# Optimization experiments

Measured on AMD Instinct MI355X. Metric: run time of the kernel, lower is better.

## Reference

```python
import jax, jax.numpy as jnp
import numpy as np

NUM_HEADS = 16
D_MODEL = 1024
D_K = D_MODEL // NUM_HEADS
B, S = 2, 2048


def setup_inputs() -> dict:
    key = jax.random.key(0)
    ks = jax.random.split(key, 10)
    q = jax.random.normal(ks[0], (B, S, D_MODEL), dtype=jnp.float32)
    k = jax.random.normal(ks[1], (B, S, D_MODEL), dtype=jnp.float32)
    v = jax.random.normal(ks[2], (B, S, D_MODEL), dtype=jnp.float32)
    # causal mask, 1 = keep, 0 = masked (masked_fill(mask==0, -1e9))
    mask = jnp.tril(jnp.ones((S, S), dtype=jnp.int32))[None, None, :, :]
    # Linear weights ~ N(0, 0.02); biases left at torch default-ish small uniform
    std = 0.02
    Wq = jax.random.normal(ks[3], (D_MODEL, D_MODEL), dtype=jnp.float32) * std
    Wk = jax.random.normal(ks[4], (D_MODEL, D_MODEL), dtype=jnp.float32) * std
    Wv = jax.random.normal(ks[5], (D_MODEL, D_MODEL), dtype=jnp.float32) * std
    bound = 1.0 / np.sqrt(D_MODEL)
    bq = jax.random.uniform(ks[6], (D_MODEL,), jnp.float32, -bound, bound)
    bk = jax.random.uniform(ks[7], (D_MODEL,), jnp.float32, -bound, bound)
    bv = jax.random.uniform(ks[8], (D_MODEL,), jnp.float32, -bound, bound)
    return {"q": q, "k": k, "v": v, "mask": mask,
            "Wq": Wq, "bq": bq, "Wk": Wk, "bk": bk, "Wv": Wv, "bv": bv}


def reference(q, k, v, mask, Wq, bq, Wk, bk, Wv, bv):
    # projections (torch Linear: x @ W.T + b), split heads -> [B, H, S, Dk]
    def proj(x, W, b):
        y = x @ W.T + b
        return y.reshape(B, S, NUM_HEADS, D_K).transpose(0, 2, 1, 3)

    qh, kh, vh = proj(q, Wq, bq), proj(k, Wk, bk), proj(v, Wv, bv)
    scores = jnp.einsum('bhqd,bhkd->bhqk', qh, kh) / jnp.sqrt(jnp.float32(D_K))
    scores = jnp.where(mask == 0, jnp.float32(-1e9), scores)
    p = jax.nn.softmax(scores, axis=-1)
    # dropout is identity in eval mode
    x = jnp.einsum('bhqk,bhkd->bhqd', p, vh)  # [B, H, S, Dk]
    return x.transpose(0, 2, 1, 3).reshape(B, S, D_MODEL)
```

## Files before the change

kernel.cpp:

```cpp
#include <hip/hip_runtime.h>

#define B_ 2
#define H_ 16
#define S_ 2048
#define DM 1024
#define DK 64
#define NX (4096 * 1024)
#define NW (1024 * 1024)

typedef unsigned short u16;
typedef __attribute__((ext_vector_type(8))) short bf16x8;
typedef __attribute__((ext_vector_type(8))) unsigned short u16x8;
typedef __attribute__((ext_vector_type(4))) unsigned short u16x4;
typedef __attribute__((ext_vector_type(4))) float f32x4;

__device__ inline u16 f2bf(float f) {
  union { float f; unsigned int u; } c; c.f = f;
  unsigned int u = c.u;
  u += 0x7fffu + ((u >> 16) & 1u);
  return (u16)(u >> 16);
}

__device__ inline u16x8 cvt8(const float* __restrict__ src) {
  const float4 a = *reinterpret_cast<const float4*>(src);
  const float4 b = *reinterpret_cast<const float4*>(src + 4);
  u16x8 r;
  r[0] = f2bf(a.x); r[1] = f2bf(a.y); r[2] = f2bf(a.z); r[3] = f2bf(a.w);
  r[4] = f2bf(b.x); r[5] = f2bf(b.y); r[6] = f2bf(b.z); r[7] = f2bf(b.w);
  return r;
}

__device__ inline void glds16(const u16* g, u16* l) {
  __builtin_amdgcn_global_load_lds(
      (const __attribute__((address_space(1))) unsigned int*)g,
      (__attribute__((address_space(3))) unsigned int*)l, 16, 0, 0);
}

__global__ __launch_bounds__(256) void cvt_kernel(
    const float* __restrict__ q, const float* __restrict__ k, const float* __restrict__ v,
    const float* __restrict__ Wq, const float* __restrict__ Wk, const float* __restrict__ Wv,
    u16* __restrict__ Xq, u16* __restrict__ Xk, u16* __restrict__ Xv,
    u16* __restrict__ Wqb, u16* __restrict__ Wkb, u16* __restrict__ Wvb)
{
  const int t = blockIdx.y;
  const float* src = (t == 0) ? q : (t == 1) ? k : (t == 2) ? v
                   : (t == 3) ? Wq : (t == 4) ? Wk : Wv;
  u16* dst = (t == 0) ? Xq : (t == 1) ? Xk : (t == 2) ? Xv
           : (t == 3) ? Wqb : (t == 4) ? Wkb : Wvb;
  const int n = (t < 3) ? NX : NW;
  const int idx = (blockIdx.x * 256 + threadIdx.x) * 8;
  if (idx >= n) return;
  *reinterpret_cast<u16x8*>(&dst[idx]) = cvt8(&src[idx]);
}

__global__ __launch_bounds__(256) void proj_kernel(
    const u16* __restrict__ Xq, const u16* __restrict__ Xk, const u16* __restrict__ Xv,
    const u16* __restrict__ Wqb, const u16* __restrict__ Wkb, const u16* __restrict__ Wvb,
    const float* __restrict__ bq, const float* __restrict__ bk, const float* __restrict__ bv,
    u16* __restrict__ Qh, u16* __restrict__ Kh, u16* __restrict__ Vh)
{
  const int z = blockIdx.z;
  const u16* X      = (z == 0) ? Xq : (z == 1) ? Xk : Xv;
  const u16* W      = (z == 0) ? Wqb : (z == 1) ? Wkb : Wvb;
  const float* bias = (z == 0) ? bq : (z == 1) ? bk : bv;
  u16* out          = (z == 0) ? Qh : (z == 1) ? Kh : Vh;
  const float scale = (z == 0) ? 0.125f : 1.0f;

  __shared__ __align__(16) u16 Xs[128 * 32];
  __shared__ __align__(16) u16 Ws[128 * 32];

  const int tid = threadIdx.x;
  const int lane = tid & 63;
  const int w = tid >> 6;
  const int wy = w >> 1, wx = w & 1;
  const int m0 = blockIdx.y * 128;
  const int n0 = blockIdx.x * 128;
  const int ml = lane & 15;
  const int qd = lane >> 4;

  f32x4 acc[4][4] = {};

  for (int kb = 0; kb < DM; kb += 32) {
    __syncthreads();
    #pragma unroll
    for (int p = 0; p < 2; ++p) {
      const int c = p * 4 + w;
      const int row = c * 16 + (lane >> 2);
      const int col = kb + (lane & 3) * 8;
      glds16(&X[(size_t)(m0 + row) * DM + col], &Xs[c * 512]);
      glds16(&W[(size_t)(n0 + row) * DM + col], &Ws[c * 512]);
    }
    __syncthreads();
    bf16x8 a[4], bfr[4];
    #pragma unroll
    for (int i = 0; i < 4; ++i)
      a[i] = *reinterpret_cast<const bf16x8*>(&Xs[(wy * 64 + i * 16 + ml) * 32 + qd * 8]);
    #pragma unroll
    for (int j = 0; j < 4; ++j)
      bfr[j] = *reinterpret_cast<const bf16x8*>(&Ws[(wx * 64 + j * 16 + ml) * 32 + qd * 8]);
    #pragma unroll
    for (int i = 0; i < 4; ++i)
      #pragma unroll
      for (int j = 0; j < 4; ++j)
        acc[i][j] = __builtin_amdgcn_mfma_f32_16x16x32_bf16(a[i], bfr[j], acc[i][j], 0, 0, 0);
  }

  #pragma unroll
  for (int j = 0; j < 4; ++j) {
    const int n = n0 + wx * 64 + j * 16 + ml;
    const float badd = bias[n];
    const int h = n >> 6, d = n & 63;
    #pragma unroll
    for (int i = 0; i < 4; ++i) {
      #pragma unroll
      for (int r = 0; r < 4; ++r) {
        const int m = m0 + wy * 64 + i * 16 + qd * 4 + r;
        const int bi = m >> 11, s = m & 2047;
        out[((bi * H_ + h) * S_ + s) * DK + d] = f2bf((acc[i][j][r] + badd) * scale);
      }
    }
  }
}

__global__ __launch_bounds__(256) void transpose_kernel(
    const u16* __restrict__ Vh, u16* __restrict__ Vt)
{
  __shared__ __align__(16) u16 T[64 * 72];
  const int t = threadIdx.x;
  const int st = blockIdx.x, bh = blockIdx.y;
  {
    const int r = t >> 2, c = (t & 3) * 16;
    const u16* src = &Vh[((size_t)bh * S_ + st * 64 + r) * DK + c];
    *reinterpret_cast<u16x8*>(&T[r * 72 + c])     = *reinterpret_cast<const u16x8*>(src);
    *reinterpret_cast<u16x8*>(&T[r * 72 + c + 8]) = *reinterpret_cast<const u16x8*>(src + 8);
  }
  __syncthreads();
  {
    const int d = t >> 2, s0 = (t & 3) * 16;
    u16x8 a, b;
    #pragma unroll
    for (int i = 0; i < 8; ++i) a[i] = T[(s0 + i) * 72 + d];
    #pragma unroll
    for (int i = 0; i < 8; ++i) b[i] = T[(s0 + 8 + i) * 72 + d];
    u16* dst = &Vt[((size_t)bh * DK + d) * S_ + st * 64 + s0];
    *reinterpret_cast<u16x8*>(dst)     = a;
    *reinterpret_cast<u16x8*>(dst + 8) = b;
  }
}

__global__ __launch_bounds__(256) void attn_kernel(
    const u16* __restrict__ Qh, const u16* __restrict__ Kh,
    const u16* __restrict__ Vt, float* __restrict__ out)
{
  __shared__ __align__(16) u16 Ks[64 * 72];
  __shared__ __align__(16) u16 Vs[64 * 72];
  __shared__ __align__(16) u16 Ps[4 * 16 * 72];

  const int tid  = threadIdx.x;
  const int lane = tid & 63;
  const int w    = tid >> 6;
  const int qt   = (gridDim.x - 1) - blockIdx.x;
  const int bh   = blockIdx.y;
  const int b    = bh >> 4, h = bh & 15;
  const int ml   = lane & 15, qd = lane >> 4;
  const int R0   = qt * 64 + w * 16;

  bf16x8 qa[2];
  #pragma unroll
  for (int ch = 0; ch < 2; ++ch)
    qa[ch] = *reinterpret_cast<const bf16x8*>(
        &Qh[((size_t)bh * S_ + R0 + ml) * DK + ch * 32 + qd * 8]);

  f32x4 oacc[4] = {};
  float l = 0.f;

  const u16* kbase = Kh + (size_t)bh * S_ * DK;
  const u16* vbase = Vt + (size_t)bh * DK * S_;
  u16* pw = &Ps[w * 16 * 72 + ml * 72];

  const int sr = tid >> 3;
  const int sc = (tid & 7) * 8;

  for (int t = 0; t <= qt; ++t) {
    __syncthreads();
    #pragma unroll
    for (int p = 0; p < 2; ++p) {
      const int r = sr + p * 32;
      *reinterpret_cast<float4*>(&Ks[r * 72 + sc]) =
          *reinterpret_cast<const float4*>(&kbase[(size_t)(t * 64 + r) * DK + sc]);
      *reinterpret_cast<float4*>(&Vs[r * 72 + sc]) =
          *reinterpret_cast<const float4*>(&vbase[(size_t)r * S_ + t * 64 + sc]);
    }
    __syncthreads();

    const bool diag = (t == qt);
    const int jmax = diag ? w : 3;

    f32x4 sfr[4];
    #pragma unroll
    for (int j = 0; j < 4; ++j) {
      if (j > jmax) break;
      f32x4 zz = {};
      #pragma unroll
      for (int ch = 0; ch < 2; ++ch) {
        bf16x8 kb = *reinterpret_cast<const bf16x8*>(&Ks[(j * 16 + ml) * 72 + ch * 32 + qd * 8]);
        zz = __builtin_amdgcn_mfma_f32_16x16x32_bf16(kb, qa[ch], zz, 0, 0, 0);
      }
      sfr[j] = zz;
    }

    if (diag) {
      #pragma unroll
      for (int r = 0; r < 4; ++r)
        if (qd * 4 + r > ml) sfr[jmax][r] = -1e30f;
    }

    #pragma unroll
    for (int j = 0; j < 4; ++j) {
      if (j <= jmax) {
        u16x4 pk;
        #pragma unroll
        for (int r = 0; r < 4; ++r) {
          const float e = __expf(sfr[j][r]);
          l += e;
          pk[r] = f2bf(e);
        }
        *reinterpret_cast<u16x4*>(&pw[j * 16 + qd * 4]) = pk;
      } else {
        *reinterpret_cast<u16x4*>(&pw[j * 16 + qd * 4]) = (u16x4){0, 0, 0, 0};
      }
    }

    const int chmax = (diag && w < 2) ? 0 : 1;
    #pragma unroll
    for (int ch = 0; ch < 2; ++ch) {
      if (ch > chmax) break;
      bf16x8 pa = *reinterpret_cast<const bf16x8*>(&Ps[w * 16 * 72 + ml * 72 + ch * 32 + qd * 8]);
      #pragma unroll
      for (int dj = 0; dj < 4; ++dj) {
        bf16x8 vb = *reinterpret_cast<const bf16x8*>(&Vs[(dj * 16 + ml) * 72 + ch * 32 + qd * 8]);
        oacc[dj] = __builtin_amdgcn_mfma_f32_16x16x32_bf16(pa, vb, oacc[dj], 0, 0, 0);
      }
    }
  }

  l += __shfl_xor(l, 16, 64);
  l += __shfl_xor(l, 32, 64);
  float lr[4];
  #pragma unroll
  for (int r = 0; r < 4; ++r) lr[r] = __shfl(l, qd * 4 + r, 64);
  #pragma unroll
  for (int dj = 0; dj < 4; ++dj)
    #pragma unroll
    for (int r = 0; r < 4; ++r) {
      const int srow = R0 + qd * 4 + r;
      out[(size_t)(b * S_ + srow) * DM + h * DK + dj * 16 + ml] = oacc[dj][r] / lr[r];
    }
}

extern "C" void kernel_launch(void* const* d_in, const int* in_sizes, int n_in,
                              void* d_out, int out_size, void* d_ws, size_t ws_size,
                              hipStream_t stream) {
  const float* q  = (const float*)d_in[0];
  const float* k  = (const float*)d_in[1];
  const float* v  = (const float*)d_in[2];
  const float* Wq = (const float*)d_in[4];
  const float* bq = (const float*)d_in[5];
  const float* Wk = (const float*)d_in[6];
  const float* bk = (const float*)d_in[7];
  const float* Wv = (const float*)d_in[8];
  const float* bv = (const float*)d_in[9];

  u16* Xq  = (u16*)d_ws;
  u16* Xk  = Xq + NX;
  u16* Xv  = Xk + NX;
  u16* Wqb = Xv + NX;
  u16* Wkb = Wqb + NW;
  u16* Wvb = Wkb + NW;
  u16* Qh  = Wvb + NW;
  u16* Kh  = Qh + NX;
  u16* Vh  = Kh + NX;
  u16* Vt  = Xq;

  cvt_kernel<<<dim3(NX / (256 * 8), 6), 256, 0, stream>>>(
      q, k, v, Wq, Wk, Wv, Xq, Xk, Xv, Wqb, Wkb, Wvb);
  proj_kernel<<<dim3(DM / 128, (B_ * S_) / 128, 3), 256, 0, stream>>>(
      Xq, Xk, Xv, Wqb, Wkb, Wvb, bq, bk, bv, Qh, Kh, Vh);
  transpose_kernel<<<dim3(S_ / 64, B_ * H_), 256, 0, stream>>>(Vh, Vt);
  attn_kernel<<<dim3(S_ / 64, B_ * H_), 256, 0, stream>>>(
      Qh, Kh, Vt, (float*)d_out);
}
```

Measured before the change: 236.3 us.

## Restructure attention with 128-row query tiles, double-buffered async K/V loads, swizzled LDS

The attention kernel now gives each block 128 query rows (two 16-row groups per wave) over a 1D grid of 512 blocks, with the block-to-(bh, tile) mapping chosen to interleave heads. K/V tiles are loaded with global_load_lds into double-buffered, XOR-swizzled LDS without padding, so the next tile's load overlaps compute. Softmax switches to exp2, with log2(e) folded into the Q scale, and uses packed bf16 conversion instructions. Work per block doubles and grid parallelism halves, and the hand-written waitcnt counts must stay consistent with the async load ordering.

```diff
diff --git a/kernel.cpp b/kernel.cpp
--- a/kernel.cpp
+++ b/kernel.cpp
@@ -12,6 +12,7 @@
 typedef __attribute__((ext_vector_type(8))) short bf16x8;
 typedef __attribute__((ext_vector_type(8))) unsigned short u16x8;
 typedef __attribute__((ext_vector_type(4))) unsigned short u16x4;
+typedef __attribute__((ext_vector_type(2))) unsigned int u32x2;
 typedef __attribute__((ext_vector_type(4))) float f32x4;
 
 __device__ inline u16 f2bf(float f) {
@@ -34,6 +35,12 @@
   __builtin_amdgcn_global_load_lds(
       (const __attribute__((address_space(1))) unsigned int*)g,
       (__attribute__((address_space(3))) unsigned int*)l, 16, 0, 0);
+}
+
+__device__ inline unsigned cvtpk(float lo, float hi) {
+  unsigned r;
+  asm("v_cvt_pk_bf16_f32 %0, %1, %2" : "=v"(r) : "v"(lo), "v"(hi));
+  return r;
 }
 
 __global__ __launch_bounds__(256) void cvt_kernel(
@@ -64,7 +71,7 @@
   const u16* W      = (z == 0) ? Wqb : (z == 1) ? Wkb : Wvb;
   const float* bias = (z == 0) ? bq : (z == 1) ? bk : bv;
   u16* out          = (z == 0) ? Qh : (z == 1) ? Kh : Vh;
-  const float scale = (z == 0) ? 0.125f : 1.0f;
+  const float scale = (z == 0) ? 0.18033688f : 1.0f;
 
   __shared__ __align__(16) u16 Xs[128 * 32];
   __shared__ __align__(16) u16 Ws[128 * 32];
@@ -152,110 +159,162 @@
     const u16* __restrict__ Qh, const u16* __restrict__ Kh,
     const u16* __restrict__ Vt, float* __restrict__ out)
 {
-  __shared__ __align__(16) u16 Ks[64 * 72];
-  __shared__ __align__(16) u16 Vs[64 * 72];
-  __shared__ __align__(16) u16 Ps[4 * 16 * 72];
+  __shared__ __align__(16) u16 Ks[2][64 * 64];
+  __shared__ __align__(16) u16 Vs[2][64 * 64];
+  __shared__ __align__(16) u16 Ps[4][2][16 * 64];
 
   const int tid  = threadIdx.x;
   const int lane = tid & 63;
   const int w    = tid >> 6;
-  const int qt   = (gridDim.x - 1) - blockIdx.x;
-  const int bh   = blockIdx.y;
-  const int b    = bh >> 4, h = bh & 15;
-  const int ml   = lane & 15, qd = lane >> 4;
-  const int R0   = qt * 64 + w * 16;
-
-  bf16x8 qa[2];
+
+  const int fid = blockIdx.x;
+  const int bh  = (fid & 7) * 4 + ((fid >> 3) & 3);
+  const int qt  = 15 - (fid >> 5);
+  const int b   = bh >> 4, h = bh & 15;
+  const int ml  = lane & 15, qd = lane >> 4;
+  const int m7  = ml & 7;
+  const int u0  = qd ^ m7;
+  const int qh  = qd >> 1, ql = qd & 1;
+  const int R0  = qt * 128;
+  const int nt  = 2 * qt + 2;
+
+  bf16x8 qa[2][2];
   #pragma unroll
-  for (int ch = 0; ch < 2; ++ch)
-    qa[ch] = *reinterpret_cast<const bf16x8*>(
-        &Qh[((size_t)bh * S_ + R0 + ml) * DK + ch * 32 + qd * 8]);
-
-  f32x4 oacc[4] = {};
-  float l = 0.f;
-
-  const u16* kbase = Kh + (size_t)bh * S_ * DK;
-  const u16* vbase = Vt + (size_t)bh * DK * S_;
-  u16* pw = &Ps[w * 16 * 72 + ml * 72];
-
-  const int sr = tid >> 3;
-  const int sc = (tid & 7) * 8;
-
-  for (int t = 0; t <= qt; ++t) {
-    __syncthreads();
-    #pragma unroll
-    for (int p = 0; p < 2; ++p) {
-      const int r = sr + p * 32;
-      *reinterpret_cast<float4*>(&Ks[r * 72 + sc]) =
-          *reinterpret_cast<const float4*>(&kbase[(size_t)(t * 64 + r) * DK + sc]);
-      *reinterpret_cast<float4*>(&Vs[r * 72 + sc]) =
-          *reinterpret_cast<const float4*>(&vbase[(size_t)r * S_ + t * 64 + sc]);
-    }
-    __syncthreads();
-
-    const bool diag = (t == qt);
-    const int jmax = diag ? w : 3;
-
-    f32x4 sfr[4];
-    #pragma unroll
-    for (int j = 0; j < 4; ++j) {
-      if (j > jmax) break;
-      f32x4 zz = {};
-      #pragma unroll
-      for (int ch = 0; ch < 2; ++ch) {
-        bf16x8 kb = *reinterpret_cast<const bf16x8*>(&Ks[(j * 16 + ml) * 72 + ch * 32 + qd * 8]);
-        zz = __builtin_amdgcn_mfma_f32_16x16x32_bf16(kb, qa[ch], zz, 0, 0, 0);
+  for (int g = 0; g < 2; ++g)
+    #pragma unroll
+    for (int ch = 0; ch < 2; ++ch)
+      qa[g][ch] = *reinterpret_cast<const bf16x8*>(
+          &Qh[((size_t)bh * S_ + R0 + w * 32 + g * 16 + ml) * DK + ch * 32 + qd * 8]);
+  asm volatile("s_waitcnt vmcnt(0)" ::: "memory");
+
+  const u16* kb0 = Kh + (size_t)bh * S_ * DK;
+  const u16* vb0 = Vt + (size_t)bh * DK * S_;
+  const int r0 = tid >> 3, r1 = r0 + 32;
+  const int cs = (tid & 7) ^ (r0 & 7);
+  const u16* sK0 = kb0 + r0 * DK + cs * 8;
+  const u16* sK1 = kb0 + r1 * DK + cs * 8;
+  const u16* sV0 = vb0 + (size_t)r0 * S_ + cs * 8;
+  const u16* sV1 = vb0 + (size_t)r1 * S_ + cs * 8;
+
+  f32x4 oacc[2][4] = {};
+  float lsum[2] = {0.f, 0.f};
+
+  glds16(sK0, &Ks[0][tid * 8]);
+  glds16(sK1, &Ks[0][2048 + tid * 8]);
+  glds16(sV0, &Vs[0][tid * 8]);
+  glds16(sV1, &Vs[0][2048 + tid * 8]);
+  sK0 += 4096; sK1 += 4096; sV0 += 64; sV1 += 64;
+
+  int cur = 0;
+  for (int t = 0; t < nt; ++t) {
+    if (t + 1 < nt) {
+      glds16(sK0, &Ks[cur ^ 1][tid * 8]);
+      glds16(sK1, &Ks[cur ^ 1][2048 + tid * 8]);
+      glds16(sV0, &Vs[cur ^ 1][tid * 8]);
+      glds16(sV1, &Vs[cur ^ 1][2048 + tid * 8]);
+      sK0 += 4096; sK1 += 4096; sV0 += 64; sV1 += 64;
+      asm volatile("s_waitcnt vmcnt(4)" ::: "memory");
+    } else {
+      asm volatile("s_waitcnt vmcnt(0)" ::: "memory");
+    }
+    __builtin_amdgcn_s_barrier();
+    asm volatile("" ::: "memory");
+
+    const u16* Kb = Ks[cur];
+    const u16* Vb = Vs[cur];
+
+    const int d16_0 = (R0 + w * 32 - t * 64) >> 4;
+    const int d16_1 = d16_0 + 1;
+    const int jtop  = (d16_1 < 3) ? d16_1 : 3;
+
+    if (jtop >= 0) {
+      #pragma unroll
+      for (int j = 0; j < 4; ++j) {
+        if (j > jtop) break;
+        const int rk = (j * 16 + ml) * 64;
+        const bf16x8 k0 = *reinterpret_cast<const bf16x8*>(&Kb[rk + u0 * 8]);
+        const bf16x8 k1 = *reinterpret_cast<const bf16x8*>(&Kb[rk + (u0 ^ 4) * 8]);
+        #pragma unroll
+        for (int g = 0; g < 2; ++g) {
+          const int d16g = d16_0 + g;
+          if (j > d16g) continue;
+          f32x4 zz = {};
+          zz = __builtin_amdgcn_mfma_f32_16x16x32_bf16(k0, qa[g][0], zz, 0, 0, 0);
+          zz = __builtin_amdgcn_mfma_f32_16x16x32_bf16(k1, qa[g][1], zz, 0, 0, 0);
+          if (j == d16g) {
+            #pragma unroll
+            for (int r = 0; r < 4; ++r)
+              if (qd * 4 + r > ml) zz[r] = -1e30f;
+          }
+          const float e0 = __builtin_amdgcn_exp2f(zz[0]);
+          const float e1 = __builtin_amdgcn_exp2f(zz[1]);
+          const float e2 = __builtin_amdgcn_exp2f(zz[2]);
+          const float e3 = __builtin_amdgcn_exp2f(zz[3]);
+          lsum[g] += (e0 + e1) + (e2 + e3);
+          u32x2 pk;
+          pk[0] = cvtpk(e0, e1);
+          pk[1] = cvtpk(e2, e3);
+          *reinterpret_cast<u32x2*>(
+              &Ps[w][g][ml * 64 + (((2 * j + qh) ^ m7) * 8) + ql * 4]) = pk;
+        }
       }
-      sfr[j] = zz;
-    }
-
-    if (diag) {
-      #pragma unroll
-      for (int r = 0; r < 4; ++r)
-        if (qd * 4 + r > ml) sfr[jmax][r] = -1e30f;
-    }
-
-    #pragma unroll
-    for (int j = 0; j < 4; ++j) {
-      if (j <= jmax) {
-        u16x4 pk;
+      #pragma unroll
+      for (int g = 0; g < 2; ++g) {
+        const int d16g = d16_0 + g;
+        if (d16g == 0 || d16g == 2) {
+          const int jz = d16g + 1;
+          *reinterpret_cast<u32x2*>(
+              &Ps[w][g][ml * 64 + (((2 * jz + qh) ^ m7) * 8) + ql * 4]) = (u32x2){0, 0};
+        }
+      }
+      #pragma unroll
+      for (int c = 0; c < 2; ++c) {
+        const bool use0 = d16_0 >= 2 * c;
+        const bool use1 = d16_1 >= 2 * c;
+        if (!(use0 | use1)) continue;
+        bf16x8 vb[4];
         #pragma unroll
-        for (int r = 0; r < 4; ++r) {
-          const float e = __expf(sfr[j][r]);
-          l += e;
-          pk[r] = f2bf(e);
+        for (int dj = 0; dj < 4; ++dj)
+          vb[dj] = *reinterpret_cast<const bf16x8*>(
+              &Vb[(dj * 16 + ml) * 64 + (u0 ^ (c << 2)) * 8]);
+        if (use0) {
+          const bf16x8 pa = *reinterpret_cast<const bf16x8*>(
+              &Ps[w][0][ml * 64 + (u0 ^ (c << 2)) * 8]);
+          #pragma unroll
+          for (int dj = 0; dj < 4; ++dj)
+            oacc[0][dj] = __builtin_amdgcn_mfma_f32_16x16x32_bf16(pa, vb[dj], oacc[0][dj], 0, 0, 0);
         }
-        *reinterpret_cast<u16x4*>(&pw[j * 16 + qd * 4]) = pk;
-      } else {
-        *reinterpret_cast<u16x4*>(&pw[j * 16 + qd * 4]) = (u16x4){0, 0, 0, 0};
+        if (use1) {
+          const bf16x8 pa = *reinterpret_cast<const bf16x8*>(
+              &Ps[w][1][ml * 64 + (u0 ^ (c << 2)) * 8]);
+          #pragma unroll
+          for (int dj = 0; dj < 4; ++dj)
+            oacc[1][dj] = __builtin_amdgcn_mfma_f32_16x16x32_bf16(pa, vb[dj], oacc[1][dj], 0, 0, 0);
+        }
       }
     }
 
-    const int chmax = (diag && w < 2) ? 0 : 1;
-    #pragma unroll
-    for (int ch = 0; ch < 2; ++ch) {
-      if (ch > chmax) break;
-      bf16x8 pa = *reinterpret_cast<const bf16x8*>(&Ps[w * 16 * 72 + ml * 72 + ch * 32 + qd * 8]);
-      #pragma unroll
-      for (int dj = 0; dj < 4; ++dj) {
-        bf16x8 vb = *reinterpret_cast<const bf16x8*>(&Vs[(dj * 16 + ml) * 72 + ch * 32 + qd * 8]);
-        oacc[dj] = __builtin_amdgcn_mfma_f32_16x16x32_bf16(pa, vb, oacc[dj], 0, 0, 0);
-      }
-    }
-  }
-
-  l += __shfl_xor(l, 16, 64);
-  l += __shfl_xor(l, 32, 64);
-  float lr[4];
+    asm volatile("" ::: "memory");
+    __builtin_amdgcn_s_barrier();
+    asm volatile("" ::: "memory");
+    cur ^= 1;
+  }
+
   #pragma unroll
-  for (int r = 0; r < 4; ++r) lr[r] = __shfl(l, qd * 4 + r, 64);
-  #pragma unroll
-  for (int dj = 0; dj < 4; ++dj)
+  for (int g = 0; g < 2; ++g) {
+    float lg = lsum[g];
+    lg += __shfl_xor(lg, 16, 64);
+    lg += __shfl_xor(lg, 32, 64);
     #pragma unroll
     for (int r = 0; r < 4; ++r) {
-      const int srow = R0 + qd * 4 + r;
-      out[(size_t)(b * S_ + srow) * DM + h * DK + dj * 16 + ml] = oacc[dj][r] / lr[r];
-    }
+      const float inv = 1.0f / __shfl(lg, qd * 4 + r, 64);
+      const int srow = R0 + w * 32 + g * 16 + qd * 4 + r;
+      float* op = &out[(size_t)(b * S_ + srow) * DM + h * DK + ml];
+      #pragma unroll
+      for (int dj = 0; dj < 4; ++dj)
+        op[dj * 16] = oacc[g][dj][r] * inv;
+    }
+  }
 }
 
 extern "C" void kernel_launch(void* const* d_in, const int* in_sizes, int n_in,
@@ -287,6 +346,6 @@
   proj_kernel<<<dim3(DM / 128, (B_ * S_) / 128, 3), 256, 0, stream>>>(
       Xq, Xk, Xv, Wqb, Wkb, Wvb, bq, bk, bv, Qh, Kh, Vh);
   transpose_kernel<<<dim3(S_ / 64, B_ * H_), 256, 0, stream>>>(Vh, Vt);
-  attn_kernel<<<dim3(S_ / 64, B_ * H_), 256, 0, stream>>>(
+  attn_kernel<<<dim3(512), 256, 0, stream>>>(
       Qh, Kh, Vt, (float*)d_out);
 }
```

After: 215.7 us. 1.1x faster.
